# Kernel tuning notes

Hardware: AMD Instinct MI355X
Metric: run time of the kernel (lower is better)

The kernel has to match this reference:

```python
import jax, jax.numpy as jnp
import numpy as np

NHEADS = 16
HEAD_DIM = 128
HIDDEN = 2048
SOFTCAP = 50.0
ROPE_BASE = 10000.0
SCALE = 256.0 ** (-0.5)  # hardcoded in original, NOT head_dim**-0.5


def _rope_tables(T, D, dtype):
    inv_freq = 1.0 / (ROPE_BASE ** (jnp.arange(0, D, 2, dtype=jnp.float32) / D))
    pos = jnp.arange(T, dtype=jnp.float32)
    freqs = pos[:, None] * inv_freq[None, :]            # [T, D/2]
    emb = jnp.concatenate([freqs, freqs], axis=-1)      # [T, D]
    # broadcast shape [1, 1, T, D] for (B, H, T, D) q/k
    return jnp.cos(emb)[None, None].astype(dtype), jnp.sin(emb)[None, None].astype(dtype)


def _rotate_half(x):
    x1, x2 = x[..., : x.shape[-1] // 2], x[..., x.shape[-1] // 2:]
    return jnp.concatenate([-x2, x1], axis=-1)


def setup_inputs() -> dict:
    key = jax.random.key(0)
    ks = jax.random.split(key, 5)
    B, T = 1, 4096
    X = jax.random.normal(ks[0], (B, T, HIDDEN), dtype=jnp.float32)
    std = 0.02
    Wq = jax.random.normal(ks[1], (HIDDEN, NHEADS * HEAD_DIM), dtype=jnp.float32) * std
    Wk = jax.random.normal(ks[2], (HIDDEN, NHEADS * HEAD_DIM), dtype=jnp.float32) * std
    Wv = jax.random.normal(ks[3], (HIDDEN, NHEADS * HEAD_DIM), dtype=jnp.float32) * std
    Wo = jax.random.normal(ks[4], (NHEADS * HEAD_DIM, HIDDEN), dtype=jnp.float32) * std
    return {"X": X, "Wq": Wq, "Wk": Wk, "Wv": Wv, "Wo": Wo}


def reference(X, Wq, Wk, Wv, Wo):
    B, T, C = X.shape
    H, D = NHEADS, HEAD_DIM
    # QKV projections -> [B, H, T, D]
    q = (X @ Wq).reshape(B, T, H, D).transpose(0, 2, 1, 3)
    k = (X @ Wk).reshape(B, T, H, D).transpose(0, 2, 1, 3)
    v = (X @ Wv).reshape(B, T, H, D).transpose(0, 2, 1, 3)
    # RoPE
    cos, sin = _rope_tables(T, D, X.dtype)
    q = q * cos + _rotate_half(q) * sin
    k = k * cos + _rotate_half(k) * sin
    # attention logits with tanh softcapping
    att = jnp.einsum("bhqd,bhkd->bhqk", q, k) * SCALE
    att = jnp.tanh(att / SOFTCAP) * SOFTCAP
    causal = jnp.tril(jnp.ones((T, T), dtype=bool))[None, None]
    att = jnp.where(causal, att, -jnp.inf)
    att = jax.nn.softmax(att, axis=-1)
    # dropout is identity (train=False)
    y = jnp.einsum("bhqk,bhkd->bhqd", att, v)
    y = y.transpose(0, 2, 1, 3).reshape(B, T, H * D)
    return y @ Wo
```

## Files before the change

### kernel.cpp

```cpp
#include <hip/hip_runtime.h>
#include <stdint.h>

#define T_SEQ 4096
#define HID   2048
#define NH    16
#define HD    128

typedef __attribute__((ext_vector_type(8))) short short8;
typedef __attribute__((ext_vector_type(4))) short short4v;
typedef __attribute__((ext_vector_type(4))) float f32x4;

typedef __attribute__((address_space(1))) void as1_void;
typedef __attribute__((address_space(3))) void as3_void;

__device__ __forceinline__ unsigned short f2bf(float f){
  unsigned u = __builtin_bit_cast(unsigned, f);
  u += 0x7fffu + ((u >> 16) & 1u);
  return (unsigned short)(u >> 16);
}
__device__ __forceinline__ float bf2f(unsigned short b){
  unsigned u = ((unsigned)b) << 16;
  return __builtin_bit_cast(float, u);
}
__device__ __forceinline__ void gll16(const void* g, void* l){
  __builtin_amdgcn_global_load_lds((as1_void*)(uintptr_t)g,
                                   (as3_void*)(unsigned)(uintptr_t)l, 16, 0, 0);
}

#define VM_WAIT(N)  asm volatile("s_waitcnt vmcnt(" #N ")" ::: "memory")
#define LGKM_WAIT0  asm volatile("s_waitcnt lgkmcnt(0)" ::: "memory")
__device__ __forceinline__ void barrier_fence(){
  asm volatile("" ::: "memory");
  __builtin_amdgcn_s_barrier();
  asm volatile("" ::: "memory");
}

__global__ __launch_bounds__(256) void conv_x_k(const float* __restrict__ X,
                                                unsigned short* __restrict__ O){
  int i = (blockIdx.x * 256 + threadIdx.x) * 4;
  float4 v = *(const float4*)(X + i);
  short4v o;
  o[0] = (short)f2bf(v.x); o[1] = (short)f2bf(v.y);
  o[2] = (short)f2bf(v.z); o[3] = (short)f2bf(v.w);
  *(short4v*)(O + i) = o;
}

__global__ __launch_bounds__(256) void conv_wt_k(const float* __restrict__ W0,
                                                 const float* __restrict__ W1,
                                                 const float* __restrict__ W2,
                                                 const float* __restrict__ W3,
                                                 unsigned short* __restrict__ Wt){
  const float* W = (blockIdx.z == 0) ? W0 : (blockIdx.z == 1) ? W1
                   : (blockIdx.z == 2) ? W2 : W3;
  unsigned short* out = Wt + (size_t)blockIdx.z * HID * HID;
  __shared__ float tile[32][33];
  const int x = threadIdx.x;
  const int y = threadIdx.y;
  const int k0 = blockIdx.y * 32, n0 = blockIdx.x * 32;
#pragma unroll
  for (int i = 0; i < 4; ++i){
    int r = y * 4 + i;
    tile[r][x] = W[(size_t)(k0 + r) * HID + n0 + x];
  }
  __syncthreads();
#pragma unroll
  for (int i = 0; i < 4; ++i){
    int r = y * 4 + i;
    out[(size_t)(n0 + r) * HID + k0 + x] = f2bf(tile[x][r]);
  }
}

template<int MODE, int NTOT>
__global__ __launch_bounds__(256, 3) void gemm_bt(
    const unsigned short* __restrict__ A,
    const unsigned short* __restrict__ Bt,
    unsigned short* __restrict__ Qb,
    unsigned short* __restrict__ Kb,
    unsigned short* __restrict__ Vt,
    float* __restrict__ Cf)
{
  constexpr int K = HID;
  __shared__ __align__(16) unsigned short lA[128 * 64];
  __shared__ __align__(16) unsigned short lB[128 * 64];

  const int tid  = threadIdx.x;
  const int wave = tid >> 6;
  const int lane = tid & 63;
  const int qd   = lane >> 4;
  const int mm   = lane & 15;
  const int m7   = mm & 7;
  const int wm   = wave >> 1;
  const int wn   = wave & 1;
  const int bm   = blockIdx.y * 128;
  const int bn   = blockIdx.x * 128;

  const unsigned short* ga[4];
  const unsigned short* gb[4];
  unsigned short* la[4];
  unsigned short* lbp[4];
#pragma unroll
  for (int i = 0; i < 4; ++i){
    int s0   = (wave * 4 + i) * 64;
    int slot = s0 + lane;
    int row  = slot >> 3;
    int kb   = (slot & 7) ^ (row & 7);
    ga[i]  = A  + (size_t)(bm + row) * K + kb * 8;
    gb[i]  = Bt + (size_t)(bn + row) * K + kb * 8;
    la[i]  = lA + s0 * 8;
    lbp[i] = lB + s0 * 8;
  }

  int abase[4], bbase[4];
#pragma unroll
  for (int t = 0; t < 4; ++t){
    abase[t] = (wm * 64 + t * 16 + mm) * 8;
    bbase[t] = (wn * 64 + t * 16 + mm) * 8;
  }

  const f32x4 fzero = {0.f, 0.f, 0.f, 0.f};
  f32x4 acc[4][4];
#pragma unroll
  for (int i = 0; i < 4; ++i)
#pragma unroll
    for (int j = 0; j < 4; ++j) acc[i][j] = fzero;

  for (int k0 = 0; k0 < K; k0 += 64){
    __syncthreads();
#pragma unroll
    for (int i = 0; i < 4; ++i){
      gll16(ga[i] + k0, la[i]);
      gll16(gb[i] + k0, lbp[i]);
    }
    __syncthreads();
#pragma unroll
    for (int ks = 0; ks < 2; ++ks){
      const int co = (ks * 4 + qd) ^ m7;
      short8 af[4], bfv[4];
#pragma unroll
      for (int t = 0; t < 4; ++t) af[t]  = *(const short8*)(lA + (abase[t] + co) * 8);
#pragma unroll
      for (int t = 0; t < 4; ++t) bfv[t] = *(const short8*)(lB + (bbase[t] + co) * 8);
#pragma unroll
      for (int i = 0; i < 4; ++i)
#pragma unroll
        for (int j = 0; j < 4; ++j)
          acc[i][j] = __builtin_amdgcn_mfma_f32_16x16x32_bf16(af[i], bfv[j], acc[i][j], 0, 0, 0);
    }
  }

#pragma unroll
  for (int i = 0; i < 4; ++i){
#pragma unroll
    for (int j = 0; j < 4; ++j){
      const int col = bn + wn * 64 + j * 16 + mm;
#pragma unroll
      for (int r = 0; r < 4; ++r){
        const int row = bm + wm * 64 + i * 16 + qd * 4 + r;
        const float v = acc[i][j][r];
        if (MODE == 0){
          const int sel = col >> 11;
          const int nn  = col & 2047;
          const int h   = nn >> 7;
          const int d   = nn & 127;
          const unsigned short bv = f2bf(v);
          if (sel == 0)      Qb[((size_t)h * T_SEQ + row) * HD + d] = bv;
          else if (sel == 1) Kb[((size_t)h * T_SEQ + row) * HD + d] = bv;
          else               Vt[((size_t)(h * HD + d)) * T_SEQ + row] = bv;
        } else {
          Cf[(size_t)row * NTOT + col] = v;
        }
      }
    }
  }
}

__global__ __launch_bounds__(256) void rope_k(unsigned short* __restrict__ Qb,
                                              unsigned short* __restrict__ Kb){
  const int j = threadIdx.x & 63;
  const int t = blockIdx.x * 4 + (threadIdx.x >> 6);
  const int h = blockIdx.y;
  const float fr = (float)t * __expf(-(float)j * (9.210340371976184f / 64.f));
  const float cs = cosf(fr), sn = sinf(fr);
  const size_t base = ((size_t)h * T_SEQ + t) * HD;
  {
    float x1 = bf2f(Qb[base + j]), x2 = bf2f(Qb[base + j + 64]);
    Qb[base + j]      = f2bf(x1 * cs - x2 * sn);
    Qb[base + j + 64] = f2bf(x2 * cs + x1 * sn);
  }
  {
    float x1 = bf2f(Kb[base + j]), x2 = bf2f(Kb[base + j + 64]);
    Kb[base + j]      = f2bf(x1 * cs - x2 * sn);
    Kb[base + j + 64] = f2bf(x2 * cs + x1 * sn);
  }
}

__global__ __launch_bounds__(256, 2) void attn_k(
    const unsigned short* __restrict__ Qb,
    const unsigned short* __restrict__ Kb,
    const unsigned short* __restrict__ Vt,
    unsigned short* __restrict__ Yb)
{
  __shared__ __align__(16) unsigned char smem[57600];
  unsigned short* lK = (unsigned short*)smem;
  unsigned short* lV = (unsigned short*)(smem + 32768);
  unsigned short (*lP)[32][32] = (unsigned short(*)[32][32])(smem + 49152);
  float* lL = (float*)(smem + 57344);
  float* lO = (float*)smem;

  const int tid  = threadIdx.x;
  const int w    = tid >> 6;
  const int rg   = w >> 1;
  const int kg   = w & 1;
  const int lane = tid & 63;
  const int qd   = lane >> 4;
  const int cc   = lane & 15;
  const int cx   = cc & 7;
  const int r8   = lane >> 3, c7 = lane & 7;

  const int b = blockIdx.x;
  const int h = (b & 7) + 8 * (b >> 8);
  const int pairP = (b >> 3) & 31;

  const int ce  = cc ^ qd;
  const int dlt = (ce & 4) ? -32 : 32;
  const unsigned short* gKbp = Kb + ((size_t)h * T_SEQ + w * 16 + qd) * HD + ce * 8;
  const int cV = c7 ^ r8;
  const unsigned short* gVbp = Vt + ((size_t)h * HD + w * 32 + r8) * T_SEQ + cV * 8;

  const f32x4 fzero = {0.f, 0.f, 0.f, 0.f};
  const float A0 = 0.0625f;
  const float A1 = -3.2552083e-8f;
  const float A2 = 2.0345052e-14f;

#pragma unroll 1
  for (int half = 0; half < 2; ++half){
    const int tp = half ? (63 - pairP) : pairP;
    const int qrow0 = tp * 64 + rg * 32;
    const int iters = tp + 1;

    {
      unsigned short* dK = lK + w * 2048;
#pragma unroll
      for (int i = 0; i < 4; ++i)
        gll16(gKbp + (size_t)(i * 4) * HD + ((i & 1) ? dlt : 0), dK + i * 512);
      unsigned short* dV = lV + w * 2048;
#pragma unroll
      for (int i = 0; i < 4; ++i)
        gll16(gVbp + (size_t)i * 8 * T_SEQ, dV + i * 512);
    }

    short8 qf[2][4];
#pragma unroll
    for (int mt = 0; mt < 2; ++mt)
#pragma unroll
      for (int ks = 0; ks < 4; ++ks)
        qf[mt][ks] = *(const short8*)(Qb + ((size_t)h * T_SEQ + qrow0 + mt * 16 + cc) * HD + ks * 32 + qd * 8);

    f32x4 o[2][8];
    float lsum[2][4];
#pragma unroll
    for (int mt = 0; mt < 2; ++mt){
#pragma unroll
      for (int dn = 0; dn < 8; ++dn) o[mt][dn] = fzero;
#pragma unroll
      for (int r = 0; r < 4; ++r) lsum[mt][r] = 0.f;
    }

    int curo = 0;
#pragma unroll 1
    for (int it = 0; it < iters; ++it){
      const int k0 = it * 64;

      if (it + 1 < iters){
        const unsigned short* gK = gKbp + (size_t)(k0 + 64) * HD;
        unsigned short* dK = lK + (curo ^ 8192) + w * 2048;
#pragma unroll
        for (int i = 0; i < 4; ++i)
          gll16(gK + (size_t)(i * 4) * HD + ((i & 1) ? dlt : 0), dK + i * 512);
        VM_WAIT(8);
      } else {
        VM_WAIT(4);
      }
      barrier_fence();

      const unsigned short* lKc = lK + curo;

      f32x4 S[2][2];
#pragma unroll
      for (int mt = 0; mt < 2; ++mt)
#pragma unroll
        for (int nt = 0; nt < 2; ++nt) S[mt][nt] = fzero;
      __builtin_amdgcn_s_setprio(1);
#pragma unroll
      for (int nt = 0; nt < 2; ++nt){
        short8 kf[4];
#pragma unroll
        for (int ks = 0; ks < 4; ++ks)
          kf[ks] = *(const short8*)(lKc + ((kg * 32 + nt * 16 + cc) * 16 + ((ks * 4 + qd) ^ cx)) * 8);
#pragma unroll
        for (int mt = 0; mt < 2; ++mt)
#pragma unroll
          for (int ks = 0; ks < 4; ++ks)
            S[mt][nt] = __builtin_amdgcn_mfma_f32_16x16x32_bf16(qf[mt][ks], kf[ks], S[mt][nt], 0, 0, 0);
      }
      __builtin_amdgcn_s_setprio(0);

      const bool domask = (it == iters - 1);
#pragma unroll
      for (int mt = 0; mt < 2; ++mt)
#pragma unroll
        for (int nt = 0; nt < 2; ++nt)
#pragma unroll
          for (int r = 0; r < 4; ++r){
            float s = S[mt][nt][r];
            float w2 = s * s;
            float t = fmaf(w2, A2, A1);
            t = fmaf(w2, t, A0);
            float a = s * t;
            a = fminf(fmaxf(a, -50.f), 50.f);
            float p = __expf(a);
            if (domask){
              int col = k0 + kg * 32 + nt * 16 + cc;
              int row = qrow0 + mt * 16 + qd * 4 + r;
              if (col > row) p = 0.f;
            }
            unsigned u = __builtin_bit_cast(unsigned, p);
            float pt = __builtin_bit_cast(float, u & 0xffff0000u);
            lsum[mt][r] += pt;
            lP[w][mt * 16 + qd * 4 + r][nt * 16 + cc] = (unsigned short)(u >> 16);
          }

      if (it + 1 < iters){
        VM_WAIT(4);
      } else {
        VM_WAIT(0);
      }
      barrier_fence();

      short8 pf[2];
#pragma unroll
      for (int mt = 0; mt < 2; ++mt)
        pf[mt] = *(const short8*)(&lP[w][mt * 16 + cc][qd * 8]);

      __builtin_amdgcn_s_setprio(1);
#pragma unroll
      for (int dn = 0; dn < 8; ++dn){
        short8 vf = *(const short8*)(lV + ((dn * 16 + cc) * 8 + ((kg * 4 + qd) ^ cx)) * 8);
#pragma unroll
        for (int mt = 0; mt < 2; ++mt)
          o[mt][dn] = __builtin_amdgcn_mfma_f32_16x16x32_bf16(pf[mt], vf, o[mt][dn], 0, 0, 0);
      }
      __builtin_amdgcn_s_setprio(0);

      LGKM_WAIT0;
      barrier_fence();

      if (it + 1 < iters){
        const unsigned short* gV = gVbp + (k0 + 64);
        unsigned short* dV = lV + w * 2048;
#pragma unroll
        for (int i = 0; i < 4; ++i)
          gll16(gV + (size_t)i * 8 * T_SEQ, dV + i * 512);
      }
      curo ^= 8192;
    }

    float lred[2][4];
#pragma unroll
    for (int mt = 0; mt < 2; ++mt)
#pragma unroll
      for (int r = 0; r < 4; ++r){
        float lb = lsum[mt][r];
        lb += __shfl_xor(lb, 1);
        lb += __shfl_xor(lb, 2);
        lb += __shfl_xor(lb, 4);
        lb += __shfl_xor(lb, 8);
        lred[mt][r] = lb;
      }

    __syncthreads();
    if (kg == 1){
#pragma unroll
      for (int mt = 0; mt < 2; ++mt){
#pragma unroll
        for (int dn = 0; dn < 8; ++dn)
          *(f32x4*)&lO[(dn * 16 + cc) * 68 + rg * 32 + mt * 16 + qd * 4] = o[mt][dn];
        if (cc == 0){
#pragma unroll
          for (int r = 0; r < 4; ++r)
            lL[rg * 32 + mt * 16 + qd * 4 + r] = lred[mt][r];
        }
      }
    }
    __syncthreads();
    if (kg == 0){
#pragma unroll
      for (int mt = 0; mt < 2; ++mt){
        float inv[4];
#pragma unroll
        for (int r = 0; r < 4; ++r){
          float lt = lred[mt][r] + lL[rg * 32 + mt * 16 + qd * 4 + r];
          inv[r] = __builtin_amdgcn_rcpf(lt);
        }
#pragma unroll
        for (int dn = 0; dn < 8; ++dn){
          f32x4 oo = o[mt][dn] + *(const f32x4*)&lO[(dn * 16 + cc) * 68 + rg * 32 + mt * 16 + qd * 4];
#pragma unroll
          for (int r = 0; r < 4; ++r){
            int row = qrow0 + mt * 16 + qd * 4 + r;
            Yb[(size_t)row * HID + h * HD + dn * 16 + cc] = f2bf(oo[r] * inv[r]);
          }
        }
      }
    }
    __syncthreads();
  }
}

extern "C" void kernel_launch(void* const* d_in, const int* in_sizes, int n_in,
                              void* d_out, int out_size, void* d_ws, size_t ws_size,
                              hipStream_t stream) {
  const float* X  = (const float*)d_in[0];
  const float* Wq = (const float*)d_in[1];
  const float* Wk = (const float*)d_in[2];
  const float* Wv = (const float*)d_in[3];
  const float* Wo = (const float*)d_in[4];
  float* out = (float*)d_out;

  unsigned short* ws = (unsigned short*)d_ws;
  unsigned short* Xb = ws;
  unsigned short* Wt = ws + (size_t)8  * 1024 * 1024;
  unsigned short* Qb = ws + (size_t)24 * 1024 * 1024;
  unsigned short* Kb = ws + (size_t)32 * 1024 * 1024;
  unsigned short* Vt = ws + (size_t)40 * 1024 * 1024;
  unsigned short* Yb = Xb;

  conv_x_k<<<8192, 256, 0, stream>>>(X, Xb);
  conv_wt_k<<<dim3(64, 64, 4), dim3(32, 8), 0, stream>>>(Wq, Wk, Wv, Wo, Wt);
  gemm_bt<0, 6144><<<dim3(48, 32), 256, 0, stream>>>(Xb, Wt, Qb, Kb, Vt, nullptr);
  rope_k<<<dim3(1024, NH), 256, 0, stream>>>(Qb, Kb);
  attn_k<<<dim3(512), 256, 0, stream>>>(Qb, Kb, Vt, Yb);
  gemm_bt<1, 2048><<<dim3(16, 32), 256, 0, stream>>>(Yb, Wt + (size_t)6144 * 2048,
                                                     nullptr, nullptr, nullptr, out);
}
```

Before: 446.2 us.

## Compute softmax row sums with MFMA against ones and use exp2 with swizzled P

Folds the log2(e) factor into the softcap polynomial so the exponential is a raw exp2 and the clamp is a single med3. The per-element row-sum accumulation and the final cross-lane shuffle reduction are replaced by an extra MFMA of the P tile against a vector of ones. The P staging buffer in LDS gets an XOR swizzle to reduce bank conflicts on writes and reads. This trades VALU work in the softmax for two extra MFMAs per iteration on the matrix pipe.

```diff
diff --git a/kernel.cpp b/kernel.cpp
--- a/kernel.cpp
+++ b/kernel.cpp
@@ -227,10 +227,17 @@
   const int cV = c7 ^ r8;
   const unsigned short* gVbp = Vt + ((size_t)h * HD + w * 32 + r8) * T_SEQ + cV * 8;
 
+  const int pc0 = (((cc >> 3)    ) ^ qd) * 8 + (cc & 7);
+  const int pc1 = (((cc >> 3) + 2) ^ qd) * 8 + (cc & 7);
+
   const f32x4 fzero = {0.f, 0.f, 0.f, 0.f};
-  const float A0 = 0.0625f;
-  const float A1 = -3.2552083e-8f;
-  const float A2 = 2.0345052e-14f;
+  const float B0 = 0.09016844006f;
+  const float B1 = -4.6962728e-8f;
+  const float B2 = 2.9351706e-14f;
+  const float CLP = 72.134752f;
+  short8 onesv;
+#pragma unroll
+  for (int j = 0; j < 8; ++j) onesv[j] = (short)0x3F80;
 
 #pragma unroll 1
   for (int half = 0; half < 2; ++half){
@@ -257,13 +264,12 @@
         qf[mt][ks] = *(const short8*)(Qb + ((size_t)h * T_SEQ + qrow0 + mt * 16 + cc) * HD + ks * 32 + qd * 8);
 
     f32x4 o[2][8];
-    float lsum[2][4];
+    f32x4 acc_l[2];
 #pragma unroll
     for (int mt = 0; mt < 2; ++mt){
 #pragma unroll
       for (int dn = 0; dn < 8; ++dn) o[mt][dn] = fzero;
-#pragma unroll
-      for (int r = 0; r < 4; ++r) lsum[mt][r] = 0.f;
+      acc_l[mt] = fzero;
     }
 
     int curo = 0;
@@ -314,20 +320,18 @@
           for (int r = 0; r < 4; ++r){
             float s = S[mt][nt][r];
             float w2 = s * s;
-            float t = fmaf(w2, A2, A1);
-            t = fmaf(w2, t, A0);
+            float t = fmaf(w2, B2, B1);
+            t = fmaf(w2, t, B0);
             float a = s * t;
-            a = fminf(fmaxf(a, -50.f), 50.f);
-            float p = __expf(a);
+            a = __builtin_amdgcn_fmed3f(a, -CLP, CLP);
+            float p = __builtin_amdgcn_exp2f(a);
             if (domask){
               int col = k0 + kg * 32 + nt * 16 + cc;
               int row = qrow0 + mt * 16 + qd * 4 + r;
               if (col > row) p = 0.f;
             }
             unsigned u = __builtin_bit_cast(unsigned, p);
-            float pt = __builtin_bit_cast(float, u & 0xffff0000u);
-            lsum[mt][r] += pt;
-            lP[w][mt * 16 + qd * 4 + r][nt * 16 + cc] = (unsigned short)(u >> 16);
+            lP[w][mt * 16 + qd * 4 + r][nt ? pc1 : pc0] = (unsigned short)(u >> 16);
           }
 
       if (it + 1 < iters){
@@ -340,7 +344,7 @@
       short8 pf[2];
 #pragma unroll
       for (int mt = 0; mt < 2; ++mt)
-        pf[mt] = *(const short8*)(&lP[w][mt * 16 + cc][qd * 8]);
+        pf[mt] = *(const short8*)(&lP[w][mt * 16 + cc][(qd ^ (cc >> 2)) * 8]);
 
       __builtin_amdgcn_s_setprio(1);
 #pragma unroll
@@ -350,6 +354,9 @@
         for (int mt = 0; mt < 2; ++mt)
           o[mt][dn] = __builtin_amdgcn_mfma_f32_16x16x32_bf16(pf[mt], vf, o[mt][dn], 0, 0, 0);
       }
+#pragma unroll
+      for (int mt = 0; mt < 2; ++mt)
+        acc_l[mt] = __builtin_amdgcn_mfma_f32_16x16x32_bf16(pf[mt], onesv, acc_l[mt], 0, 0, 0);
       __builtin_amdgcn_s_setprio(0);
 
       LGKM_WAIT0;
@@ -365,19 +372,6 @@
       curo ^= 8192;
     }
 
-    float lred[2][4];
-#pragma unroll
-    for (int mt = 0; mt < 2; ++mt)
-#pragma unroll
-      for (int r = 0; r < 4; ++r){
-        float lb = lsum[mt][r];
-        lb += __shfl_xor(lb, 1);
-        lb += __shfl_xor(lb, 2);
-        lb += __shfl_xor(lb, 4);
-        lb += __shfl_xor(lb, 8);
-        lred[mt][r] = lb;
-      }
-
     __syncthreads();
     if (kg == 1){
 #pragma unroll
@@ -388,7 +382,7 @@
         if (cc == 0){
 #pragma unroll
           for (int r = 0; r < 4; ++r)
-            lL[rg * 32 + mt * 16 + qd * 4 + r] = lred[mt][r];
+            lL[rg * 32 + mt * 16 + qd * 4 + r] = acc_l[mt][r];
         }
       }
     }
@@ -399,7 +393,7 @@
         float inv[4];
 #pragma unroll
         for (int r = 0; r < 4; ++r){
-          float lt = lred[mt][r] + lL[rg * 32 + mt * 16 + qd * 4 + r];
+          float lt = acc_l[mt][r] + lL[rg * 32 + mt * 16 + qd * 4 + r];
           inv[r] = __builtin_amdgcn_rcpf(lt);
         }
 #pragma unroll
```

Result: no change. 441.0 us (-1.2%).
